# Kernel optimization log

Hardware: AMD Instinct MI355X
Metric: run time of the kernel (lower is better)

## Reference

```python
import jax, jax.numpy as jnp
import numpy as np

B, L, D = 4096, 16, 256  # batch, feat_len, feat_dim
N_ENC = 2                # common + synergy encoders


def _layer_norm(x, gamma, beta, eps=1e-5):
    m = jnp.mean(x, axis=-1, keepdims=True)
    v = jnp.mean(jnp.square(x - m), axis=-1, keepdims=True)
    return (x - m) * jax.lax.rsqrt(v + eps) * gamma + beta


def _estimator(gin, pin, Wg, bg, gng, gnb, Wp, bp, png, pnb, wga, bga, wpa, bpa):
    # MLP_Block = Linear + LayerNorm (Dropout is identity at inference)
    g = _layer_norm(jnp.einsum('bld,ed->ble', gin, Wg) + bg, gng, gnb)  # [B,L,D]
    p = _layer_norm(jnp.einsum('bld,ed->ble', pin, Wp) + bp, png, pnb)  # [B,L,D]
    # atten[b,l,i,j] = g[b,l,i]*p[b,l,j]
    # Linear(D,1) over j: sum_j wga_j*g_i*p_j + bga = g_i*(p.wga) + bga  (fused, no [B,L,D,D])
    geno_att = jax.nn.sigmoid(g * jnp.einsum('bld,d->bl', p, wga)[..., None] + bga)
    # permuted copy: atten.T over last two dims, Linear over i: p_j*(g.wpa) + bpa
    path_att = jax.nn.sigmoid(p * jnp.einsum('bld,d->bl', g, wpa)[..., None] + bpa)
    return p * path_att + g * geno_att


def setup_inputs() -> dict:
    key = jax.random.key(0)
    ks = jax.random.split(key, 8)
    s = 1.0 / np.sqrt(D)
    inp = {
        'gfeat': jax.random.normal(ks[0], (B, L, D), jnp.float32),
        'pfeat': jax.random.normal(ks[1], (B, L, D), jnp.float32),
        # stacked params for the 2 encoders (common, synergy)
        'Wg': jax.random.normal(ks[2], (N_ENC, D, D), jnp.float32) * s,
        'bg': jnp.zeros((N_ENC, D), jnp.float32),
        'gng': jnp.ones((N_ENC, D), jnp.float32),
        'gnb': jnp.zeros((N_ENC, D), jnp.float32),
        'Wp': jax.random.normal(ks[3], (N_ENC, D, D), jnp.float32) * s,
        'bp': jnp.zeros((N_ENC, D), jnp.float32),
        'png': jnp.ones((N_ENC, D), jnp.float32),
        'pnb': jnp.zeros((N_ENC, D), jnp.float32),
        'wga': jax.random.normal(ks[4], (N_ENC, D), jnp.float32) * s,
        'bga': jnp.zeros((N_ENC,), jnp.float32),
        'wpa': jax.random.normal(ks[5], (N_ENC, D), jnp.float32) * s,
        'bpa': jnp.zeros((N_ENC,), jnp.float32),
    }
    return inp


def reference(gfeat, pfeat, Wg, bg, gng, gnb, Wp, bp, png, pnb, wga, bga, wpa, bpa):
    # Knowledge_Decomposition calls both encoders as encoder(pfeat, gfeat) (swapped)
    est = jax.vmap(_estimator, in_axes=(None, None) + (0,) * 12)
    out = est(pfeat, gfeat, Wg, bg, gng, gnb, Wp, bp, png, pnb, wga, bga, wpa, bpa)  # [2,B,L,D]
    return (out[0], out[1])  # (common, synergy)
```

## Files before the change

kernel.cpp:

```cpp
#include <hip/hip_runtime.h>
#include <stdint.h>

typedef __bf16 bf16x8 __attribute__((ext_vector_type(8)));
typedef float  f32x4  __attribute__((ext_vector_type(4)));

#define BLD   16777216
#define DDIM  256

#define AG_OFF    0
#define AP_OFF    16384
#define PARAM_OFF 32768
#define STATS_OFF 40960
#define ROWC_OFF  45056
#define CONST_OFF 46080
#define SMEM_BYTES 46096

__device__ __forceinline__ float sigmoid_fast(float x){
  float e = __builtin_amdgcn_exp2f(-1.44269504f * x);
  return __builtin_amdgcn_rcpf(1.0f + e);
}

__device__ __forceinline__ bf16x8 cvt8(const float* p){
  float4 a = *(const float4*)p;
  float4 b = *(const float4*)(p + 4);
  bf16x8 r;
  r[0]=(__bf16)a.x; r[1]=(__bf16)a.y; r[2]=(__bf16)a.z; r[3]=(__bf16)a.w;
  r[4]=(__bf16)b.x; r[5]=(__bf16)b.y; r[6]=(__bf16)b.z; r[7]=(__bf16)b.w;
  return r;
}

__device__ __forceinline__ float ldp(const unsigned char* sm, int arr, int col){
  return ((const float*)(sm + PARAM_OFF))[arr*256 + col];
}

__global__ __launch_bounds__(256, 3)
void kd_kernel(const float* __restrict__ gfeat, const float* __restrict__ pfeat,
               const float* __restrict__ Wg,  const float* __restrict__ bg,
               const float* __restrict__ gng, const float* __restrict__ gnb,
               const float* __restrict__ Wp,  const float* __restrict__ bp,
               const float* __restrict__ pngm,const float* __restrict__ pnb,
               const float* __restrict__ wga, const float* __restrict__ bga,
               const float* __restrict__ wpa, const float* __restrict__ bpa,
               float* __restrict__ out)
{
  __shared__ __align__(16) unsigned char sm[SMEM_BYTES];
  const int tid  = threadIdx.x;
  const int n    = tid & 15;
  const int q    = (tid >> 4) & 3;
  const int w    = tid >> 6;
  const int tile = blockIdx.x >> 1;
  const int e    = blockIdx.x & 1;

  const int q16  = q*16;
  const int xorv = (n & 7) << 4;

  {
    float* pp = (float*)(sm + PARAM_OFF);
    pp[0*256 + tid] = bg  [e*256 + tid];
    pp[1*256 + tid] = gng [e*256 + tid];
    pp[2*256 + tid] = gnb [e*256 + tid];
    pp[3*256 + tid] = bp  [e*256 + tid];
    pp[4*256 + tid] = pngm[e*256 + tid];
    pp[5*256 + tid] = pnb [e*256 + tid];
    pp[6*256 + tid] = wga [e*256 + tid];
    pp[7*256 + tid] = wpa [e*256 + tid];
  }

  {
    const float* srcG = pfeat + (size_t)tile*32*DDIM;
    const float* srcP = gfeat + (size_t)tile*32*DDIM;
    #pragma unroll
    for (int j = 0; j < 4; ++j){
      int idx = j*2048 + tid*8;
      int row = idx >> 8;
      int col = idx & 255;
      bf16x8 vg = cvt8(srcG + idx);
      bf16x8 vp = cvt8(srcP + idx);
      int off = row*512 + ((col*2) ^ ((row & 7) << 4));
      *(bf16x8*)(sm + AG_OFF + off) = vg;
      *(bf16x8*)(sm + AP_OFF + off) = vp;
    }
  }
  __syncthreads();

  if (tid < 64){
    float c0=0.f, c1=0.f, c2=0.f, c3=0.f;
    #pragma unroll
    for (int j = 0; j < 4; ++j){
      int c = tid*4 + j;
      float gng_ = ldp(sm,1,c), gnb_ = ldp(sm,2,c);
      float png_ = ldp(sm,4,c), pnb_ = ldp(sm,5,c);
      float wga_ = ldp(sm,6,c), wpa_ = ldp(sm,7,c);
      c0 += gng_*wpa_; c1 += gnb_*wpa_; c2 += png_*wga_; c3 += pnb_*wga_;
    }
    #pragma unroll
    for (int m = 1; m <= 32; m <<= 1){
      c0 += __shfl_xor(c0,m); c1 += __shfl_xor(c1,m);
      c2 += __shfl_xor(c2,m); c3 += __shfl_xor(c3,m);
    }
    if (tid == 0){
      float* cp = (float*)(sm + CONST_OFF);
      cp[0]=c0; cp[1]=c1; cp[2]=c2; cp[3]=c3;
    }
  }

  f32x4 accg[2][4], accp[2][4];
  #pragma unroll
  for (int t = 0; t < 4; ++t){
    int col = w*64 + n*4 + t;
    float bgv = ldp(sm,0,col);
    float bpv = ldp(sm,3,col);
    #pragma unroll
    for (int s = 0; s < 2; ++s){
      accg[s][t] = (f32x4){bgv,bgv,bgv,bgv};
      accp[s][t] = (f32x4){bpv,bpv,bpv,bpv};
    }
  }

  const float* wgE = Wg + (size_t)e*65536;
  const float* wpE = Wp + (size_t)e*65536;
  int woff[4];
  #pragma unroll
  for (int t = 0; t < 4; ++t)
    woff[t] = (w*64 + n*4 + t)*DDIM + q*8;

  for (int kk = 0; kk < 8; ++kk){
    bf16x8 aG[2], aP[2], bG[4], bP[4];
    #pragma unroll
    for (int s = 0; s < 2; ++s){
      int off = (s*16 + n)*512 + ((kk*64 + q16) ^ xorv);
      aG[s] = *(const bf16x8*)(sm + AG_OFF + off);
      aP[s] = *(const bf16x8*)(sm + AP_OFF + off);
    }
    #pragma unroll
    for (int t = 0; t < 4; ++t){
      bG[t] = cvt8(wgE + woff[t] + kk*32);
      bP[t] = cvt8(wpE + woff[t] + kk*32);
    }
    #pragma unroll
    for (int s = 0; s < 2; ++s){
      #pragma unroll
      for (int t = 0; t < 4; ++t){
        accg[s][t] = __builtin_amdgcn_mfma_f32_16x16x32_bf16(aG[s], bG[t], accg[s][t], 0,0,0);
        accp[s][t] = __builtin_amdgcn_mfma_f32_16x16x32_bf16(aP[s], bP[t], accp[s][t], 0,0,0);
      }
    }
  }

  float gamg[4], betg[4], gamp[4], betp[4], gwk[4], pwk[4];
  #pragma unroll
  for (int t = 0; t < 4; ++t){
    int col = w*64 + n*4 + t;
    float gng_ = ldp(sm,1,col), gnb_ = ldp(sm,2,col);
    float png_ = ldp(sm,4,col), pnb_ = ldp(sm,5,col);
    float wga_ = ldp(sm,6,col), wpa_ = ldp(sm,7,col);
    gamg[t]=gng_; betg[t]=gnb_; gamp[t]=png_; betp[t]=pnb_;
    gwk[t]=gng_*wpa_;
    pwk[t]=png_*wga_;
  }

  #pragma unroll
  for (int s = 0; s < 2; ++s){
    #pragma unroll
    for (int reg = 0; reg < 4; ++reg){
      float gs=0.f,gq=0.f,gw=0.f,ps=0.f,pq=0.f,pw=0.f;
      #pragma unroll
      for (int t = 0; t < 4; ++t){
        float xg = accg[s][t][reg], xp = accp[s][t][reg];
        gs += xg; gq = fmaf(xg,xg,gq); gw = fmaf(xg,gwk[t],gw);
        ps += xp; pq = fmaf(xp,xp,pq); pw = fmaf(xp,pwk[t],pw);
      }
      #pragma unroll
      for (int m = 1; m <= 8; m <<= 1){
        gs += __shfl_xor(gs,m); gq += __shfl_xor(gq,m); gw += __shfl_xor(gw,m);
        ps += __shfl_xor(ps,m); pq += __shfl_xor(pq,m); pw += __shfl_xor(pw,m);
      }
      if (n == 0){
        int r = s*16 + q*4 + reg;
        float* st = (float*)(sm + STATS_OFF) + (r*4 + w)*8;
        st[0]=gs; st[1]=gq; st[2]=gw; st[3]=ps; st[4]=pq; st[5]=pw;
      }
    }
  }
  __syncthreads();

  if (tid < 32){
    const float* cs = (const float*)(sm + CONST_OFF);
    float gs=0.f,gq=0.f,gw=0.f,ps=0.f,pq=0.f,pw=0.f;
    #pragma unroll
    for (int w2 = 0; w2 < 4; ++w2){
      const float* st = (const float*)(sm + STATS_OFF) + (tid*4 + w2)*8;
      gs+=st[0]; gq+=st[1]; gw+=st[2]; ps+=st[3]; pq+=st[4]; pw+=st[5];
    }
    float mg = gs*(1.f/256.f), vg = fmaxf(gq*(1.f/256.f) - mg*mg, 0.f);
    float rsg = rsqrtf(vg + 1e-5f);
    float mp = ps*(1.f/256.f), vp = fmaxf(pq*(1.f/256.f) - mp*mp, 0.f);
    float rsp = rsqrtf(vp + 1e-5f);
    float sp = rsg*(gw - mg*cs[0]) + cs[1];
    float sg = rsp*(pw - mp*cs[2]) + cs[3];
    float* rc = (float*)(sm + ROWC_OFF) + tid*8;
    rc[0]=mg; rc[1]=rsg; rc[2]=mp; rc[3]=rsp; rc[4]=sg; rc[5]=sp;
  }
  __syncthreads();

  const float bgaf = bga[e];
  const float bpaf = bpa[e];
  #pragma unroll
  for (int s = 0; s < 2; ++s){
    #pragma unroll
    for (int reg = 0; reg < 4; ++reg){
      int r = s*16 + q*4 + reg;
      const float* rc = (const float*)(sm + ROWC_OFF) + r*8;
      float mg=rc[0], rsg=rc[1], mp=rc[2], rsp=rc[3], sg=rc[4], sp=rc[5];
      float4 o;
      float ov[4];
      #pragma unroll
      for (int t = 0; t < 4; ++t){
        float g_ln = fmaf((accg[s][t][reg]-mg)*rsg, gamg[t], betg[t]);
        float p_ln = fmaf((accp[s][t][reg]-mp)*rsp, gamp[t], betp[t]);
        float ga = sigmoid_fast(fmaf(g_ln, sg, bgaf));
        float pa = sigmoid_fast(fmaf(p_ln, sp, bpaf));
        ov[t] = p_ln*pa + g_ln*ga;
      }
      o.x = ov[0]; o.y = ov[1]; o.z = ov[2]; o.w = ov[3];
      size_t off = (size_t)e*BLD + ((size_t)tile*32 + r)*DDIM + (w*64 + n*4);
      *(float4*)(out + off) = o;
    }
  }
}

extern "C" void kernel_launch(void* const* d_in, const int* in_sizes, int n_in,
                              void* d_out, int out_size, void* d_ws, size_t ws_size,
                              hipStream_t stream) {
  const float* gfeat = (const float*)d_in[0];
  const float* pfeat = (const float*)d_in[1];
  const float* Wg    = (const float*)d_in[2];
  const float* bg    = (const float*)d_in[3];
  const float* gng   = (const float*)d_in[4];
  const float* gnb   = (const float*)d_in[5];
  const float* Wp    = (const float*)d_in[6];
  const float* bp    = (const float*)d_in[7];
  const float* pngm  = (const float*)d_in[8];
  const float* pnb   = (const float*)d_in[9];
  const float* wga   = (const float*)d_in[10];
  const float* bga   = (const float*)d_in[11];
  const float* wpa   = (const float*)d_in[12];
  const float* bpa   = (const float*)d_in[13];

  dim3 grid(4096), block(256);
  hipLaunchKernelGGL(kd_kernel, grid, block, 0, stream,
                     gfeat, pfeat, Wg, bg, gng, gnb, Wp, bp, pngm, pnb,
                     wga, bga, wpa, bpa, (float*)d_out);
}
```

Baseline: 453.6 us.

## Make kernel persistent with register-resident weights and double-buffered input tiles

Switches to 256 persistent blocks of 512 threads. Each block loops over 16 row tiles, and warps are split so that half handle the G matrix and half the P matrix. The bf16 weight fragments are loaded once into registers and reused across all tiles instead of being re-read from global memory per tile. The next tile's inputs are prefetched into a double-buffered LDS slab while the current tile is computed. Per-row stats and the cross-matrix combine now go through LDS exchange buffers, which adds more barriers per tile, raises register pressure from the weight fragments, and leaves only 256 blocks to fill the device.

```diff
diff --git a/kernel.cpp b/kernel.cpp
--- a/kernel.cpp
+++ b/kernel.cpp
@@ -6,34 +6,37 @@
 
 #define BLD   16777216
 #define DDIM  256
-
-#define AG_OFF    0
-#define AP_OFF    16384
-#define PARAM_OFF 32768
-#define STATS_OFF 40960
-#define ROWC_OFF  45056
-#define CONST_OFF 46080
-#define SMEM_BYTES 46096
+#define NT    16
+
+#define ABUF_OFF  0
+#define PARAM_OFF 65536
+#define STATS_OFF 73728
+#define ROWC_OFF  78336
+#define CONST_OFF 79488
+#define EXG_OFF   79504
+#define EXP_OFF   96144
+#define SMEM_BYTES 112784
 
 __device__ __forceinline__ float sigmoid_fast(float x){
   float e = __builtin_amdgcn_exp2f(-1.44269504f * x);
   return __builtin_amdgcn_rcpf(1.0f + e);
 }
 
-__device__ __forceinline__ bf16x8 cvt8(const float* p){
-  float4 a = *(const float4*)p;
-  float4 b = *(const float4*)(p + 4);
+__device__ __forceinline__ bf16x8 pack8(float4 a, float4 b){
   bf16x8 r;
   r[0]=(__bf16)a.x; r[1]=(__bf16)a.y; r[2]=(__bf16)a.z; r[3]=(__bf16)a.w;
   r[4]=(__bf16)b.x; r[5]=(__bf16)b.y; r[6]=(__bf16)b.z; r[7]=(__bf16)b.w;
   return r;
 }
+__device__ __forceinline__ bf16x8 cvt8(const float* p){
+  return pack8(*(const float4*)p, *(const float4*)(p+4));
+}
 
 __device__ __forceinline__ float ldp(const unsigned char* sm, int arr, int col){
   return ((const float*)(sm + PARAM_OFF))[arr*256 + col];
 }
 
-__global__ __launch_bounds__(256, 3)
+__global__ __launch_bounds__(512, 2)
 void kd_kernel(const float* __restrict__ gfeat, const float* __restrict__ pfeat,
                const float* __restrict__ Wg,  const float* __restrict__ bg,
                const float* __restrict__ gng, const float* __restrict__ gnb,
@@ -48,13 +51,19 @@
   const int n    = tid & 15;
   const int q    = (tid >> 4) & 3;
   const int w    = tid >> 6;
-  const int tile = blockIdx.x >> 1;
+  const int mat  = w >> 2;
+  const int wq   = w & 3;
   const int e    = blockIdx.x & 1;
+  const int b2   = blockIdx.x >> 1;
 
   const int q16  = q*16;
   const int xorv = (n & 7) << 4;
-
-  {
+  const int colb = wq*64 + n*4;
+
+  const float* srcG = pfeat;
+  const float* srcP = gfeat;
+
+  if (tid < 256){
     float* pp = (float*)(sm + PARAM_OFF);
     pp[0*256 + tid] = bg  [e*256 + tid];
     pp[1*256 + tid] = gng [e*256 + tid];
@@ -66,20 +75,20 @@
     pp[7*256 + tid] = wpa [e*256 + tid];
   }
 
+  const int sofs = tid*16;
+  const int srow = sofs >> 8, scol = sofs & 255;
+  const int sb0  = srow*512 + (( scol    *2) ^ ((srow & 7) << 4));
+  const int sb1  = srow*512 + (((scol+8) *2) ^ ((srow & 7) << 4));
+
   {
-    const float* srcG = pfeat + (size_t)tile*32*DDIM;
-    const float* srcP = gfeat + (size_t)tile*32*DDIM;
-    #pragma unroll
-    for (int j = 0; j < 4; ++j){
-      int idx = j*2048 + tid*8;
-      int row = idx >> 8;
-      int col = idx & 255;
-      bf16x8 vg = cvt8(srcG + idx);
-      bf16x8 vp = cvt8(srcP + idx);
-      int off = row*512 + ((col*2) ^ ((row & 7) << 4));
-      *(bf16x8*)(sm + AG_OFF + off) = vg;
-      *(bf16x8*)(sm + AP_OFF + off) = vp;
-    }
+    const float* g0 = srcG + (size_t)(b2*NT)*8192 + sofs;
+    const float* p0 = srcP + (size_t)(b2*NT)*8192 + sofs;
+    float4 a0=*(const float4*)(g0), a1=*(const float4*)(g0+4), a2=*(const float4*)(g0+8), a3=*(const float4*)(g0+12);
+    float4 c0=*(const float4*)(p0), c1=*(const float4*)(p0+4), c2=*(const float4*)(p0+8), c3=*(const float4*)(p0+12);
+    *(bf16x8*)(sm + sb0)         = pack8(a0,a1);
+    *(bf16x8*)(sm + sb1)         = pack8(a2,a3);
+    *(bf16x8*)(sm + 16384 + sb0) = pack8(c0,c1);
+    *(bf16x8*)(sm + 16384 + sb1) = pack8(c2,c3);
   }
   __syncthreads();
 
@@ -104,128 +113,156 @@
     }
   }
 
-  f32x4 accg[2][4], accp[2][4];
+  const float* wsrc = (mat ? Wp : Wg) + (size_t)e*65536;
+  bf16x8 wf[8][4];
   #pragma unroll
-  for (int t = 0; t < 4; ++t){
-    int col = w*64 + n*4 + t;
-    float bgv = ldp(sm,0,col);
-    float bpv = ldp(sm,3,col);
+  for (int kk = 0; kk < 8; ++kk)
+    #pragma unroll
+    for (int t = 0; t < 4; ++t)
+      wf[kk][t] = cvt8(wsrc + (size_t)(colb + t)*DDIM + kk*32 + q*8);
+
+  const float* pp = (const float*)(sm + PARAM_OFF);
+  float4 biasv = *(const float4*)(pp + (mat?3:0)*256 + colb);
+  float4 gamv  = *(const float4*)(pp + (mat?4:1)*256 + colb);
+  float4 betv  = *(const float4*)(pp + (mat?5:2)*256 + colb);
+  float4 wav   = *(const float4*)(pp + (mat?6:7)*256 + colb);
+  float wk[4];
+  wk[0]=((float*)&gamv)[0]*((float*)&wav)[0]; wk[1]=((float*)&gamv)[1]*((float*)&wav)[1];
+  wk[2]=((float*)&gamv)[2]*((float*)&wav)[2]; wk[3]=((float*)&gamv)[3]*((float*)&wav)[3];
+  const float attb = mat ? bpa[e] : bga[e];
+
+  int cur = 0;
+  float4 pfG[4], pfP[4];
+
+  for (int i = 0; i < NT; ++i){
+    const int tile = b2*NT + i;
+
+    f32x4 acc[2][4];
+    #pragma unroll
+    for (int t = 0; t < 4; ++t){
+      float bv = ((const float*)&biasv)[t];
+      acc[0][t] = (f32x4){bv,bv,bv,bv};
+      acc[1][t] = (f32x4){bv,bv,bv,bv};
+    }
+
+    {
+      const unsigned char* slab = sm + cur*32768 + mat*16384;
+      #pragma unroll
+      for (int kk = 0; kk < 8; ++kk){
+        int co = (kk*64 + q16) ^ xorv;
+        bf16x8 a0 = *(const bf16x8*)(slab + (n     )*512 + co);
+        bf16x8 a1 = *(const bf16x8*)(slab + (16 + n)*512 + co);
+        #pragma unroll
+        for (int t = 0; t < 4; ++t){
+          acc[0][t] = __builtin_amdgcn_mfma_f32_16x16x32_bf16(a0, wf[kk][t], acc[0][t], 0,0,0);
+          acc[1][t] = __builtin_amdgcn_mfma_f32_16x16x32_bf16(a1, wf[kk][t], acc[1][t], 0,0,0);
+        }
+      }
+    }
+
+    if (i+1 < NT){
+      const float* gN = srcG + (size_t)(tile+1)*8192 + sofs;
+      const float* pN = srcP + (size_t)(tile+1)*8192 + sofs;
+      #pragma unroll
+      for (int v = 0; v < 4; ++v){
+        pfG[v] = *(const float4*)(gN + v*4);
+        pfP[v] = *(const float4*)(pN + v*4);
+      }
+    }
+
     #pragma unroll
     for (int s = 0; s < 2; ++s){
-      accg[s][t] = (f32x4){bgv,bgv,bgv,bgv};
-      accp[s][t] = (f32x4){bpv,bpv,bpv,bpv};
-    }
-  }
-
-  const float* wgE = Wg + (size_t)e*65536;
-  const float* wpE = Wp + (size_t)e*65536;
-  int woff[4];
-  #pragma unroll
-  for (int t = 0; t < 4; ++t)
-    woff[t] = (w*64 + n*4 + t)*DDIM + q*8;
-
-  for (int kk = 0; kk < 8; ++kk){
-    bf16x8 aG[2], aP[2], bG[4], bP[4];
-    #pragma unroll
-    for (int s = 0; s < 2; ++s){
-      int off = (s*16 + n)*512 + ((kk*64 + q16) ^ xorv);
-      aG[s] = *(const bf16x8*)(sm + AG_OFF + off);
-      aP[s] = *(const bf16x8*)(sm + AP_OFF + off);
-    }
-    #pragma unroll
-    for (int t = 0; t < 4; ++t){
-      bG[t] = cvt8(wgE + woff[t] + kk*32);
-      bP[t] = cvt8(wpE + woff[t] + kk*32);
-    }
-    #pragma unroll
-    for (int s = 0; s < 2; ++s){
-      #pragma unroll
-      for (int t = 0; t < 4; ++t){
-        accg[s][t] = __builtin_amdgcn_mfma_f32_16x16x32_bf16(aG[s], bG[t], accg[s][t], 0,0,0);
-        accp[s][t] = __builtin_amdgcn_mfma_f32_16x16x32_bf16(aP[s], bP[t], accp[s][t], 0,0,0);
-      }
-    }
-  }
-
-  float gamg[4], betg[4], gamp[4], betp[4], gwk[4], pwk[4];
-  #pragma unroll
-  for (int t = 0; t < 4; ++t){
-    int col = w*64 + n*4 + t;
-    float gng_ = ldp(sm,1,col), gnb_ = ldp(sm,2,col);
-    float png_ = ldp(sm,4,col), pnb_ = ldp(sm,5,col);
-    float wga_ = ldp(sm,6,col), wpa_ = ldp(sm,7,col);
-    gamg[t]=gng_; betg[t]=gnb_; gamp[t]=png_; betp[t]=pnb_;
-    gwk[t]=gng_*wpa_;
-    pwk[t]=png_*wga_;
-  }
-
-  #pragma unroll
-  for (int s = 0; s < 2; ++s){
-    #pragma unroll
-    for (int reg = 0; reg < 4; ++reg){
+      #pragma unroll
+      for (int reg = 0; reg < 4; ++reg){
+        float xs=0.f, xq=0.f, xw=0.f;
+        #pragma unroll
+        for (int t = 0; t < 4; ++t){
+          float x = acc[s][t][reg];
+          xs += x; xq = fmaf(x,x,xq); xw = fmaf(x,wk[t],xw);
+        }
+        #pragma unroll
+        for (int m = 1; m <= 8; m <<= 1){
+          xs += __shfl_xor(xs,m); xq += __shfl_xor(xq,m); xw += __shfl_xor(xw,m);
+        }
+        if (n == 0){
+          int r = s*16 + q*4 + reg;
+          float4 st = {xs, xq, xw, 0.f};
+          *(float4*)(sm + STATS_OFF + r*144 + (wq*2 + mat)*16) = st;
+        }
+      }
+    }
+    __syncthreads();
+
+    if (i+1 < NT){
+      unsigned char* dst = sm + (cur^1)*32768;
+      *(bf16x8*)(dst + sb0)         = pack8(pfG[0],pfG[1]);
+      *(bf16x8*)(dst + sb1)         = pack8(pfG[2],pfG[3]);
+      *(bf16x8*)(dst + 16384 + sb0) = pack8(pfP[0],pfP[1]);
+      *(bf16x8*)(dst + 16384 + sb1) = pack8(pfP[2],pfP[3]);
+    }
+
+    if (tid < 32){
+      const float* cs = (const float*)(sm + CONST_OFF);
       float gs=0.f,gq=0.f,gw=0.f,ps=0.f,pq=0.f,pw=0.f;
       #pragma unroll
-      for (int t = 0; t < 4; ++t){
-        float xg = accg[s][t][reg], xp = accp[s][t][reg];
-        gs += xg; gq = fmaf(xg,xg,gq); gw = fmaf(xg,gwk[t],gw);
-        ps += xp; pq = fmaf(xp,xp,pq); pw = fmaf(xp,pwk[t],pw);
-      }
-      #pragma unroll
-      for (int m = 1; m <= 8; m <<= 1){
-        gs += __shfl_xor(gs,m); gq += __shfl_xor(gq,m); gw += __shfl_xor(gw,m);
-        ps += __shfl_xor(ps,m); pq += __shfl_xor(pq,m); pw += __shfl_xor(pw,m);
-      }
-      if (n == 0){
+      for (int w2 = 0; w2 < 4; ++w2){
+        float4 sg_ = *(const float4*)(sm + STATS_OFF + tid*144 + (w2*2  )*16);
+        float4 sp_ = *(const float4*)(sm + STATS_OFF + tid*144 + (w2*2+1)*16);
+        gs+=sg_.x; gq+=sg_.y; gw+=sg_.z;
+        ps+=sp_.x; pq+=sp_.y; pw+=sp_.z;
+      }
+      float mg = gs*(1.f/256.f), vg = fmaxf(gq*(1.f/256.f) - mg*mg, 0.f);
+      float rsg = rsqrtf(vg + 1e-5f);
+      float mp = ps*(1.f/256.f), vp = fmaxf(pq*(1.f/256.f) - mp*mp, 0.f);
+      float rsp = rsqrtf(vp + 1e-5f);
+      float sp = rsg*(gw - mg*cs[0]) + cs[1];
+      float sg = rsp*(pw - mp*cs[2]) + cs[3];
+      float* rc = (float*)(sm + ROWC_OFF) + tid*9;
+      rc[0]=mg; rc[1]=rsg; rc[2]=mp; rc[3]=rsp; rc[4]=sg; rc[5]=sp;
+    }
+    __syncthreads();
+
+    {
+      const int s = 1 - mat;
+      #pragma unroll
+      for (int reg = 0; reg < 4; ++reg){
         int r = s*16 + q*4 + reg;
-        float* st = (float*)(sm + STATS_OFF) + (r*4 + w)*8;
-        st[0]=gs; st[1]=gq; st[2]=gw; st[3]=ps; st[4]=pq; st[5]=pw;
-      }
-    }
-  }
-  __syncthreads();
-
-  if (tid < 32){
-    const float* cs = (const float*)(sm + CONST_OFF);
-    float gs=0.f,gq=0.f,gw=0.f,ps=0.f,pq=0.f,pw=0.f;
-    #pragma unroll
-    for (int w2 = 0; w2 < 4; ++w2){
-      const float* st = (const float*)(sm + STATS_OFF) + (tid*4 + w2)*8;
-      gs+=st[0]; gq+=st[1]; gw+=st[2]; ps+=st[3]; pq+=st[4]; pw+=st[5];
-    }
-    float mg = gs*(1.f/256.f), vg = fmaxf(gq*(1.f/256.f) - mg*mg, 0.f);
-    float rsg = rsqrtf(vg + 1e-5f);
-    float mp = ps*(1.f/256.f), vp = fmaxf(pq*(1.f/256.f) - mp*mp, 0.f);
-    float rsp = rsqrtf(vp + 1e-5f);
-    float sp = rsg*(gw - mg*cs[0]) + cs[1];
-    float sg = rsp*(pw - mp*cs[2]) + cs[3];
-    float* rc = (float*)(sm + ROWC_OFF) + tid*8;
-    rc[0]=mg; rc[1]=rsg; rc[2]=mp; rc[3]=rsp; rc[4]=sg; rc[5]=sp;
-  }
-  __syncthreads();
-
-  const float bgaf = bga[e];
-  const float bpaf = bpa[e];
-  #pragma unroll
-  for (int s = 0; s < 2; ++s){
-    #pragma unroll
-    for (int reg = 0; reg < 4; ++reg){
-      int r = s*16 + q*4 + reg;
-      const float* rc = (const float*)(sm + ROWC_OFF) + r*8;
-      float mg=rc[0], rsg=rc[1], mp=rc[2], rsp=rc[3], sg=rc[4], sp=rc[5];
-      float4 o;
-      float ov[4];
-      #pragma unroll
-      for (int t = 0; t < 4; ++t){
-        float g_ln = fmaf((accg[s][t][reg]-mg)*rsg, gamg[t], betg[t]);
-        float p_ln = fmaf((accp[s][t][reg]-mp)*rsp, gamp[t], betp[t]);
-        float ga = sigmoid_fast(fmaf(g_ln, sg, bgaf));
-        float pa = sigmoid_fast(fmaf(p_ln, sp, bpaf));
-        ov[t] = p_ln*pa + g_ln*ga;
-      }
-      o.x = ov[0]; o.y = ov[1]; o.z = ov[2]; o.w = ov[3];
-      size_t off = (size_t)e*BLD + ((size_t)tile*32 + r)*DDIM + (w*64 + n*4);
-      *(float4*)(out + off) = o;
-    }
+        const float* rc = (const float*)(sm + ROWC_OFF) + r*9;
+        float mean = rc[mat*2], rs = rc[mat*2+1], srow = rc[4+mat];
+        float4 cv;
+        #pragma unroll
+        for (int t = 0; t < 4; ++t){
+          float ln = fmaf((acc[s][t][reg]-mean)*rs, ((const float*)&gamv)[t], ((const float*)&betv)[t]);
+          ((float*)&cv)[t] = ln * sigmoid_fast(fmaf(ln, srow, attb));
+        }
+        int off = mat ? (EXP_OFF + r*1040) : (EXG_OFF + (r-16)*1040);
+        *(float4*)(sm + off + colb*4) = cv;
+      }
+    }
+    __syncthreads();
+
+    {
+      const int s = mat;
+      #pragma unroll
+      for (int reg = 0; reg < 4; ++reg){
+        int r = s*16 + q*4 + reg;
+        const float* rc = (const float*)(sm + ROWC_OFF) + r*9;
+        float mean = rc[mat*2], rs = rc[mat*2+1], srow = rc[4+mat];
+        int off = mat ? (EXG_OFF + (r-16)*1040) : (EXP_OFF + r*1040);
+        float4 pc = *(const float4*)(sm + off + colb*4);
+        float4 o;
+        #pragma unroll
+        for (int t = 0; t < 4; ++t){
+          float ln = fmaf((acc[s][t][reg]-mean)*rs, ((const float*)&gamv)[t], ((const float*)&betv)[t]);
+          float cown = ln * sigmoid_fast(fmaf(ln, srow, attb));
+          ((float*)&o)[t] = mat ? (cown + ((const float*)&pc)[t])
+                                : (((const float*)&pc)[t] + cown);
+        }
+        *(float4*)(out + (size_t)e*BLD + ((size_t)tile*32 + r)*DDIM + colb) = o;
+      }
+    }
+    __syncthreads();
+    cur ^= 1;
   }
 }
 
@@ -247,7 +284,7 @@
   const float* wpa   = (const float*)d_in[12];
   const float* bpa   = (const float*)d_in[13];
 
-  dim3 grid(4096), block(256);
+  dim3 grid(256), block(512);
   hipLaunchKernelGGL(kd_kernel, grid, block, 0, stream,
                      gfeat, pfeat, Wg, bg, gng, gnb, Wp, bp, pngm, pnb,
                      wga, bga, wpa, bpa, (float*)d_out);
```

After: 573.2 us. 1.26x slower.
